# Kernel tuning notes

Hardware: AMD Instinct MI355X
Metric: run time of the kernel (lower is better)

Reference implementation:

```python
import jax, jax.numpy as jnp
import numpy as np

EPS = 1e-5
NUM_HEADS = 16

def rmsnorm(x, w=None, eps=EPS):
    y = x * jax.lax.rsqrt(jnp.mean(x * x, axis=-1, keepdims=True) + eps)
    return y if w is None else y * w

def act_quant(x):
    # per-token 8-bit absmax activation quantization (BitNet b1.58)
    scale = 127.0 / jnp.clip(jnp.max(jnp.abs(x), axis=-1, keepdims=True), 1e-5, None)
    return jnp.clip(jnp.round(x * scale), -128, 127) / scale

def weight_quant(w):
    # ternary (1.58-bit) absmean weight quantization
    scale = 1.0 / jnp.clip(jnp.mean(jnp.abs(w)), 1e-5, None)
    return jnp.clip(jnp.round(w * scale), -1, 1) / scale

def bit_linear(x, w):
    # BitLinear: RMSNorm -> STE-quantized activation @ STE-quantized ternary weight
    xn = rmsnorm(x)
    xq = xn + jax.lax.stop_gradient(act_quant(xn) - xn)
    wq = w + jax.lax.stop_gradient(weight_quant(w) - w)
    return xq @ wq.T

def hgrn_recurrence(i, logf):
    # elementwise gated linear recurrence: h_t = exp(logf_t) * h_{t-1} + i_t
    def step(h, xs):
        ii, ff = xs
        h = jnp.exp(ff) * h + ii
        return h, h
    B, T, D = i.shape
    _, o = jax.lax.scan(step, jnp.zeros((B, D), i.dtype),
                        (jnp.swapaxes(i, 0, 1), jnp.swapaxes(logf, 0, 1)))
    return jnp.swapaxes(o, 0, 1)  # [B, T, D]

def hgrn_bit_attention(x, w_i, w_f, w_g, w_o, g_norm_w):
    i = bit_linear(x, w_i)
    f = bit_linear(x, w_f)
    logf = jax.nn.log_sigmoid(f)
    i = jax.nn.silu(i) * (1.0 - jax.nn.sigmoid(f))  # swiglu(i, 1 - sigmoid(f))
    o = hgrn_recurrence(i, logf)
    g = bit_linear(x, w_g)
    B, T, D = o.shape
    oh = rmsnorm(o.reshape(B, T, NUM_HEADS, D // NUM_HEADS), g_norm_w)  # per-head RMSNorm
    o = oh.reshape(B, T, D) * g * jax.nn.sigmoid(g)  # swish gate (FusedRMSNormSwishGate)
    return bit_linear(o, w_o)

def setup_inputs() -> dict:
    key = jax.random.key(0)
    B, S_S, S_C, D = 4, 4096, 512, 2048
    ks = jax.random.split(key, 16)
    mk = lambda k: jax.random.normal(k, (D, D), jnp.float32) * 0.02
    return {
        "hidden_states": jax.random.normal(ks[0], (B, S_S, D), jnp.float32),
        "encoder_hidden_states": jax.random.normal(ks[1], (B, S_C, D), jnp.float32),
        "w_q": mk(ks[2]), "w_k": mk(ks[3]), "w_v": mk(ks[4]), "w_out": mk(ks[5]),
        "w_add_q": mk(ks[6]), "w_add_k": mk(ks[7]), "w_add_v": mk(ks[8]), "w_add_out": mk(ks[9]),
        "w_i": mk(ks[10]), "w_f": mk(ks[11]), "w_g": mk(ks[12]), "w_o": mk(ks[13]),
        "g_norm_w": jnp.ones((D // NUM_HEADS,), jnp.float32),
    }

def reference(hidden_states, encoder_hidden_states, w_q, w_k, w_v, w_out,
              w_add_q, w_add_k, w_add_v, w_add_out, w_i, w_f, w_g, w_o, g_norm_w):
    q_s = bit_linear(hidden_states, w_q)
    k_s = bit_linear(hidden_states, w_k)          # computed as in original; unused by attn
    v_s = bit_linear(hidden_states, w_v)          # computed as in original; unused by attn
    q_c = bit_linear(encoder_hidden_states, w_add_q)
    k_c = bit_linear(encoder_hidden_states, w_add_k)
    v_c = bit_linear(encoder_hidden_states, w_add_v)
    q_joint = jnp.concatenate([q_c, q_s], axis=1)  # context first, then stream
    attn_out = hgrn_bit_attention(q_joint, w_i, w_f, w_g, w_o, g_norm_w)
    len_c = encoder_hidden_states.shape[1]
    out_c, out_s = attn_out[:, :len_c, :], attn_out[:, len_c:, :]
    return (bit_linear(out_s, w_out), bit_linear(out_c, w_add_out))
```

## Files before the change

kernel.cpp:

```cpp
#include <hip/hip_runtime.h>
#include <math.h>
#include <stdint.h>

#define D2 2048

typedef int v4i __attribute__((ext_vector_type(4)));
typedef int v16i __attribute__((ext_vector_type(16)));

struct Ptrs8 { const float* p[8]; };
struct RowMap { int seg, jump, off; };

enum { QW_Q = 0, QW_OUT = 1, QW_ADDQ = 2, QW_ADDOUT = 3, QW_I = 4, QW_F = 5, QW_G = 6, QW_O = 7 };

__device__ __forceinline__ int rmap(RowMap m, int r) {
  return (r / m.seg) * m.jump + (r % m.seg) + m.off;
}

__device__ __forceinline__ void gload16(const void* g, void* l) {
  __builtin_amdgcn_global_load_lds((__attribute__((address_space(1))) void*)g,
                                   (__attribute__((address_space(3))) void*)l, 16, 0, 0);
}

__device__ __forceinline__ float fsig(float x) {
  return __builtin_amdgcn_rcpf(1.0f + __expf(-x));
}

__device__ __forceinline__ void gswz(int nM, int& mb, int& nb) {
  int bid = blockIdx.x;
  int wg = (bid & 7) * (nM << 1) + (bid >> 3);
  mb = wg >> 4;
  nb = wg & 15;
}

__global__ __launch_bounds__(256) void k_wabs(Ptrs8 wsrc, double* part) {
  int m = blockIdx.y;
  const float4* w4 = (const float4*)(wsrc.p[m] + (size_t)blockIdx.x * 4096 + threadIdx.x * 16);
  double s = 0.0;
#pragma unroll
  for (int j = 0; j < 4; ++j) {
    float4 v = w4[j];
    s += (double)fabsf(v.x) + (double)fabsf(v.y) + (double)fabsf(v.z) + (double)fabsf(v.w);
  }
#pragma unroll
  for (int o = 32; o; o >>= 1) s += __shfl_down(s, o);
  __shared__ double red[4];
  if ((threadIdx.x & 63) == 0) red[threadIdx.x >> 6] = s;
  __syncthreads();
  if (threadIdx.x == 0) part[(size_t)m * 1024 + blockIdx.x] = red[0] + red[1] + red[2] + red[3];
}

__global__ __launch_bounds__(256) void k_wmean(const double* part, double* wqs, float* wmul) {
  int m = blockIdx.x, t = threadIdx.x;
  const double* p = part + (size_t)m * 1024;
  double s = p[t] + p[t + 256] + p[t + 512] + p[t + 768];
#pragma unroll
  for (int o = 32; o; o >>= 1) s += __shfl_down(s, o);
  __shared__ double red[4];
  if ((t & 63) == 0) red[t >> 6] = s;
  __syncthreads();
  if (t == 0) {
    double mean = (red[0] + red[1] + red[2] + red[3]) * (1.0 / 4194304.0);
    double cl = mean > 1e-5 ? mean : 1e-5;
    wqs[m] = 1.0 / cl;
    wmul[m] = (float)cl;
  }
}

__global__ __launch_bounds__(256) void k_wquant(Ptrs8 wsrc, const double* wqs, int8_t* wq) {
  int m = blockIdx.y;
  double qs = wqs[m];
  size_t base = (size_t)blockIdx.x * 4096 + threadIdx.x * 16;
  const float4* w4 = (const float4*)(wsrc.p[m] + base);
  union { int8_t b[16]; int4 v; } u;
#pragma unroll
  for (int j = 0; j < 4; ++j) {
    float4 v = w4[j];
    float f[4] = {v.x, v.y, v.z, v.w};
#pragma unroll
    for (int c = 0; c < 4; ++c) {
      int q = (int)rint((double)f[c] * qs);
      q = q > 1 ? 1 : (q < -1 ? -1 : q);
      u.b[j * 4 + c] = (int8_t)q;
    }
  }
  *(int4*)(wq + (size_t)m * 4194304 + base) = u.v;
}

__global__ __launch_bounds__(256) void k_actq(const float* __restrict__ x, int8_t* __restrict__ q,
                                              float* __restrict__ inv) {
  int row = blockIdx.x, t = threadIdx.x;
  const float4* xr = (const float4*)(x + (size_t)row * D2);
  float4 a = xr[t * 2], b = xr[t * 2 + 1];
  float v[8] = {a.x, a.y, a.z, a.w, b.x, b.y, b.z, b.w};
  float ss = 0.f, ma = 0.f;
#pragma unroll
  for (int j = 0; j < 8; ++j) { ss += v[j] * v[j]; ma = fmaxf(ma, fabsf(v[j])); }
#pragma unroll
  for (int o = 32; o; o >>= 1) { ss += __shfl_down(ss, o); ma = fmaxf(ma, __shfl_down(ma, o)); }
  __shared__ float rs[4], rm[4], bc[2];
  if ((t & 63) == 0) { rs[t >> 6] = ss; rm[t >> 6] = ma; }
  __syncthreads();
  if (t == 0) {
    float S = rs[0] + rs[1] + rs[2] + rs[3];
    float M = fmaxf(fmaxf(rm[0], rm[1]), fmaxf(rm[2], rm[3]));
    float r = 1.0f / sqrtf(S * (1.0f / 2048.0f) + 1e-5f);
    float mx = fmaxf(M * r, 1e-5f);
    bc[0] = r;
    bc[1] = 127.0f / mx;
    inv[row] = mx * (1.0f / 127.0f);
  }
  __syncthreads();
  float r = bc[0], s = bc[1];
  union { int8_t b8[8]; int2 p2; } u;
#pragma unroll
  for (int j = 0; j < 8; ++j) {
    float xn = v[j] * r;
    int qq = (int)rintf(xn * s);
    qq = qq > 127 ? 127 : (qq < -128 ? -128 : qq);
    u.b8[j] = (int8_t)qq;
  }
  ((int2*)(q + (size_t)row * D2))[t] = u.p2;
}

#define SYNC_PIPE(N)                                          \
  do {                                                        \
    __builtin_amdgcn_sched_barrier(0);                        \
    asm volatile("s_waitcnt vmcnt(" #N ")" ::: "memory");     \
    __builtin_amdgcn_sched_barrier(0);                        \
    __builtin_amdgcn_s_barrier();                             \
    __builtin_amdgcn_sched_barrier(0);                        \
  } while (0)

__device__ __forceinline__ void gemm_mainloop(const int8_t* __restrict__ Aq,
                                              const int8_t* __restrict__ Wq, int ga0, int ga1,
                                              int n0, int t, int8_t* lds, v16i acc[2][2]) {
  const int wid = t >> 6, lane = t & 63;
  const int wr = wid >> 1, wc = wid & 1, am = lane & 31, g = lane >> 5;
  const int arow = t >> 2;
  const int achk = ((t & 3) ^ ((arow >> 1) & 3)) * 16;
  const int8_t* agp0 = Aq + (size_t)ga0 * 2048 + achk;
  const int8_t* agp1 = Aq + (size_t)ga1 * 2048 + achk;
  const int8_t* bgp0 = Wq + (size_t)(n0 + arow) * 2048 + achk;
  const int8_t* bgp1 = Wq + (size_t)(n0 + 64 + arow) * 2048 + achk;
  int8_t* A0 = lds;
  int8_t* B0 = lds + 8192;
  int8_t* A1 = lds + 16384;
  int8_t* B1 = lds + 24576;
  int8_t* A2 = lds + 32768;
  int8_t* B2 = lds + 40960;

#define STAGE(Ab, Bb)                                 \
  do {                                                \
    gload16(agp0, (Ab) + wid * 1024);                 \
    gload16(agp1, (Ab) + 4096 + wid * 1024);          \
    gload16(bgp0, (Bb) + wid * 1024);                 \
    gload16(bgp1, (Bb) + 4096 + wid * 1024);          \
    agp0 += 64; agp1 += 64; bgp0 += 64; bgp1 += 64;   \
  } while (0)

#define COMPUTE(Ab, Bb)                                                                     \
  do {                                                                                      \
    _Pragma("unroll") for (int kk = 0; kk < 2; ++kk) {                                      \
      v4i af[2], bf[2];                                                                     \
      _Pragma("unroll") for (int mi = 0; mi < 2; ++mi) {                                    \
        int r = wr * 64 + mi * 32 + am;                                                     \
        int slot = ((kk << 1) | g) ^ ((r >> 1) & 3);                                        \
        af[mi] = *(const v4i*)((Ab) + r * 64 + slot * 16);                                  \
        int rb = wc * 64 + mi * 32 + am;                                                    \
        int slotb = ((kk << 1) | g) ^ ((rb >> 1) & 3);                                      \
        bf[mi] = *(const v4i*)((Bb) + rb * 64 + slotb * 16);                                \
      }                                                                                     \
      _Pragma("unroll") for (int mi = 0; mi < 2; ++mi)                                      \
        _Pragma("unroll") for (int ni = 0; ni < 2; ++ni)                                    \
          acc[mi][ni] =                                                                     \
              __builtin_amdgcn_mfma_i32_32x32x32_i8(af[mi], bf[ni], acc[mi][ni], 0, 0, 0);  \
    }                                                                                       \
  } while (0)

  STAGE(A0, B0);
  STAGE(A1, B1);
  STAGE(A2, B2);
  SYNC_PIPE(8);
#pragma unroll 1
  for (int tt = 0; tt < 30; tt += 3) {
    COMPUTE(A0, B0);
    SYNC_PIPE(4);
    if (tt + 3 < 32) STAGE(A0, B0);
    COMPUTE(A1, B1);
    SYNC_PIPE(4);
    if (tt + 4 < 32) STAGE(A1, B1);
    COMPUTE(A2, B2);
    SYNC_PIPE(4);
    if (tt + 5 < 32) STAGE(A2, B2);
  }
  COMPUTE(A0, B0);
  SYNC_PIPE(0);
  COMPUTE(A1, B1);
#undef STAGE
#undef COMPUTE
}

__global__ __launch_bounds__(256) void k_gemm(const int8_t* __restrict__ Aq,
                                              const float* __restrict__ ainv,
                                              const int8_t* __restrict__ Wq,
                                              const float* __restrict__ wmul, int widx,
                                              float* __restrict__ C, RowMap inm, RowMap outm,
                                              int nM) {
  __shared__ __align__(16) int8_t lds[49152];
  int mb, nb;
  gswz(nM, mb, nb);
  int m0 = mb * 128, n0 = nb * 128;
  int t = threadIdx.x;
  int lane = t & 63, wid = t >> 6;
  int wr = wid >> 1, wc = wid & 1;
  int am = lane & 31, g = lane >> 5;
  int ga0 = rmap(inm, m0 + (t >> 2));
  int ga1 = rmap(inm, m0 + 64 + (t >> 2));

  v16i acc[2][2] = {};
  gemm_mainloop(Aq, Wq, ga0, ga1, n0, t, lds, acc);

  float wm = wmul[widx];
#pragma unroll
  for (int mi = 0; mi < 2; ++mi) {
#pragma unroll
    for (int q = 0; q < 16; ++q) {
      int rin = wr * 64 + mi * 32 + (q & 3) + ((q >> 2) * 8) + g * 4;
      int ra = rmap(inm, m0 + rin);
      int rc = rmap(outm, m0 + rin);
      float s = ainv[ra] * wm;
#pragma unroll
      for (int ni = 0; ni < 2; ++ni) {
        C[(size_t)rc * 2048 + n0 + wc * 64 + ni * 32 + am] = (float)acc[mi][ni][q] * s;
      }
    }
  }
}

__global__ __launch_bounds__(256) void k_gemm_f(const int8_t* __restrict__ Aq,
                                                const float* __restrict__ ainv,
                                                const int8_t* __restrict__ Wq,
                                                const float* __restrict__ wmul,
                                                float* __restrict__ IG, float* __restrict__ AD,
                                                int nM) {
  __shared__ __align__(16) int8_t lds[49152];
  int mb, nb;
  gswz(nM, mb, nb);
  int m0 = mb * 128, n0 = nb * 128;
  int t = threadIdx.x;
  int lane = t & 63, wid = t >> 6;
  int wr = wid >> 1, wc = wid & 1;
  int am = lane & 31, g = lane >> 5;
  int ga0 = m0 + (t >> 2);
  int ga1 = m0 + 64 + (t >> 2);

  v16i acc[2][2] = {};
  gemm_mainloop(Aq, Wq, ga0, ga1, n0, t, lds, acc);

  float wm = wmul[QW_F];
#pragma unroll
  for (int mi = 0; mi < 2; ++mi) {
#pragma unroll
    for (int q = 0; q < 16; ++q) {
      int rin = m0 + wr * 64 + mi * 32 + (q & 3) + ((q >> 2) * 8) + g * 4;
      float s = ainv[rin] * wm;
#pragma unroll
      for (int ni = 0; ni < 2; ++ni) {
        size_t idx = (size_t)rin * 2048 + n0 + wc * 64 + ni * 32 + am;
        float fval = (float)acc[mi][ni][q] * s;
        float iv = IG[idx];
        float a = fsig(fval);
        float si = iv * fsig(iv);
        IG[idx] = si * (1.0f - a);
        AD[idx] = a;
      }
    }
  }
}

__global__ __launch_bounds__(256) void k_rec1(const float* __restrict__ ig,
                                              const float* __restrict__ ad,
                                              float* __restrict__ chA, float* __restrict__ chH) {
  int tid = blockIdx.x * 256 + threadIdx.x;
  int chain = tid & 8191;
  int c = tid >> 13;
  int b = chain >> 11, d = chain & 2047;
  size_t base = ((size_t)b * 4608 + (size_t)c * 72) * 2048 + d;
  float h = 0.f, P = 1.f;
  for (int s = 0; s < 72; ++s) {
    float av = ad[base];
    float iv = ig[base];
    h = av * h + iv;
    P *= av;
    base += 2048;
  }
  chA[(size_t)c * 8192 + chain] = P;
  chH[(size_t)c * 8192 + chain] = h;
}

__global__ __launch_bounds__(256) void k_rec2(const float* __restrict__ chA,
                                              const float* __restrict__ chH,
                                              float* __restrict__ chC) {
  int chain = blockIdx.x * 256 + threadIdx.x;
  float carry = 0.f;
  for (int c = 0; c < 64; ++c) {
    chC[(size_t)c * 8192 + chain] = carry;
    carry = chA[(size_t)c * 8192 + chain] * carry + chH[(size_t)c * 8192 + chain];
  }
}

__global__ __launch_bounds__(256) void k_rec3(float* __restrict__ io, const float* __restrict__ ad,
                                              const float* __restrict__ chC) {
  int tid = blockIdx.x * 256 + threadIdx.x;
  int chain = tid & 8191;
  int c = tid >> 13;
  int b = chain >> 11, d = chain & 2047;
  size_t base = ((size_t)b * 4608 + (size_t)c * 72) * 2048 + d;
  float h = chC[(size_t)c * 8192 + chain];
  for (int s = 0; s < 72; ++s) {
    float av = ad[base];
    float iv = io[base];
    h = av * h + iv;
    io[base] = h;
    base += 2048;
  }
}

__global__ __launch_bounds__(256) void k_hnq(const float* __restrict__ o,
                                             const float* __restrict__ g,
                                             const float* __restrict__ gnw,
                                             int8_t* __restrict__ q, float* __restrict__ inv) {
  int row = blockIdx.x, t = threadIdx.x;
  size_t base = (size_t)row * D2 + (size_t)t * 8;
  float4 a = *(const float4*)(o + base);
  float4 b = *(const float4*)(o + base + 4);
  float v[8] = {a.x, a.y, a.z, a.w, b.x, b.y, b.z, b.w};
  float ss = 0.f;
#pragma unroll
  for (int j = 0; j < 8; ++j) ss += v[j] * v[j];
  ss += __shfl_xor(ss, 1);
  ss += __shfl_xor(ss, 2);
  ss += __shfl_xor(ss, 4);
  ss += __shfl_xor(ss, 8);
  float r = 1.0f / sqrtf(ss * (1.0f / 128.0f) + 1e-5f);
  float4 ga = *(const float4*)(g + base);
  float4 gb = *(const float4*)(g + base + 4);
  float gv[8] = {ga.x, ga.y, ga.z, ga.w, gb.x, gb.y, gb.z, gb.w};
  int j0 = (t & 15) * 8;
  float o2[8];
#pragma unroll
  for (int j = 0; j < 8; ++j) {
    float gg = gv[j];
    o2[j] = v[j] * r * gnw[j0 + j] * gg * fsig(gg);
  }
  float ss2 = 0.f, ma = 0.f;
#pragma unroll
  for (int j = 0; j < 8; ++j) { ss2 += o2[j] * o2[j]; ma = fmaxf(ma, fabsf(o2[j])); }
#pragma unroll
  for (int off = 32; off; off >>= 1) {
    ss2 += __shfl_down(ss2, off);
    ma = fmaxf(ma, __shfl_down(ma, off));
  }
  __shared__ float rs[4], rm[4], bc[2];
  if ((t & 63) == 0) { rs[t >> 6] = ss2; rm[t >> 6] = ma; }
  __syncthreads();
  if (t == 0) {
    float S = rs[0] + rs[1] + rs[2] + rs[3];
    float M = fmaxf(fmaxf(rm[0], rm[1]), fmaxf(rm[2], rm[3]));
    float rr = 1.0f / sqrtf(S * (1.0f / 2048.0f) + 1e-5f);
    float mx = fmaxf(M * rr, 1e-5f);
    bc[0] = rr;
    bc[1] = 127.0f / mx;
    inv[row] = mx * (1.0f / 127.0f);
  }
  __syncthreads();
  float rr = bc[0], s = bc[1];
  union { int8_t b8[8]; int2 p2; } u;
#pragma unroll
  for (int j = 0; j < 8; ++j) {
    float xn = o2[j] * rr;
    int qq = (int)rintf(xn * s);
    qq = qq > 127 ? 127 : (qq < -128 ? -128 : qq);
    u.b8[j] = (int8_t)qq;
  }
  ((int2*)(q + (size_t)row * D2))[t] = u.p2;
}

extern "C" void kernel_launch(void* const* d_in, const int* in_sizes, int n_in,
                              void* d_out, int out_size, void* d_ws, size_t ws_size,
                              hipStream_t stream) {
  const float* hid = (const float*)d_in[0];
  const float* enc = (const float*)d_in[1];
  const float* gnw = (const float*)d_in[14];
  Ptrs8 wp;
  wp.p[QW_Q] = (const float*)d_in[2];
  wp.p[QW_OUT] = (const float*)d_in[5];
  wp.p[QW_ADDQ] = (const float*)d_in[6];
  wp.p[QW_ADDOUT] = (const float*)d_in[9];
  wp.p[QW_I] = (const float*)d_in[10];
  wp.p[QW_F] = (const float*)d_in[11];
  wp.p[QW_G] = (const float*)d_in[12];
  wp.p[QW_O] = (const float*)d_in[13];
  float* out = (float*)d_out;

  char* ws = (char*)d_ws;
  float* bufA = (float*)ws;
  float* bufB = bufA + 37748736;
  int8_t* actq = (int8_t*)(bufB + 37748736);
  int8_t* wq = actq + 37748736;
  float* ainv = (float*)(wq + 33554432);
  double* wpart = (double*)(ainv + 18432);
  double* wqs = wpart + 8192;
  float* wmul = (float*)(wqs + 8);
  float* chA = wmul + 8;
  float* chH = chA + 524288;
  float* chC = chH + 524288;
  if (ws_size < 379723872ULL) return;

  RowMap idm{0x40000000, 0, 0};
  RowMap seqm{4096, 4608, 512};
  RowMap encm{512, 4608, 0};

  k_wabs<<<dim3(1024, 8), 256, 0, stream>>>(wp, wpart);
  k_wmean<<<8, 256, 0, stream>>>(wpart, wqs, wmul);
  k_wquant<<<dim3(1024, 8), 256, 0, stream>>>(wp, wqs, wq);
  k_actq<<<16384, 256, 0, stream>>>(hid, actq, ainv);
  k_actq<<<2048, 256, 0, stream>>>(enc, actq + (size_t)16384 * 2048, ainv + 16384);
  k_gemm<<<128 * 16, 256, 0, stream>>>(actq, ainv, wq + (size_t)QW_Q * 4194304, wmul, QW_Q,
                                       bufA, idm, seqm, 128);
  k_gemm<<<16 * 16, 256, 0, stream>>>(actq + (size_t)16384 * 2048, ainv + 16384,
                                      wq + (size_t)QW_ADDQ * 4194304, wmul, QW_ADDQ, bufA,
                                      idm, encm, 16);
  k_actq<<<18432, 256, 0, stream>>>(bufA, actq, ainv);
  k_gemm<<<144 * 16, 256, 0, stream>>>(actq, ainv, wq + (size_t)QW_I * 4194304, wmul, QW_I,
                                       bufA, idm, idm, 144);
  k_gemm<<<144 * 16, 256, 0, stream>>>(actq, ainv, wq + (size_t)QW_G * 4194304, wmul, QW_G,
                                       out, idm, idm, 144);
  k_gemm_f<<<144 * 16, 256, 0, stream>>>(actq, ainv, wq + (size_t)QW_F * 4194304, wmul,
                                         bufA, bufB, 144);
  k_rec1<<<2048, 256, 0, stream>>>(bufA, bufB, chA, chH);
  k_rec2<<<32, 256, 0, stream>>>(chA, chH, chC);
  k_rec3<<<2048, 256, 0, stream>>>(bufA, bufB, chC);
  k_hnq<<<18432, 256, 0, stream>>>(bufA, out, gnw, actq, ainv);
  k_gemm<<<144 * 16, 256, 0, stream>>>(actq, ainv, wq + (size_t)QW_O * 4194304, wmul, QW_O,
                                       bufB, idm, idm, 144);
  k_actq<<<18432, 256, 0, stream>>>(bufB, actq, ainv);
  k_gemm<<<128 * 16, 256, 0, stream>>>(actq, ainv, wq + (size_t)QW_OUT * 4194304, wmul,
                                       QW_OUT, out, seqm, idm, 128);
  k_gemm<<<16 * 16, 256, 0, stream>>>(actq, ainv, wq + (size_t)QW_ADDOUT * 4194304, wmul,
                                      QW_ADDOUT, out + (size_t)33554432, encm, idm, 16);
}
```

Baseline: 1.117 ms.

## Use 256x256 int8 MFMA GEMM tiles with 512-thread blocks for large projections

Adds a 256x256-tile int8 GEMM with 8 waves per block, a double-buffered 64-deep K pipeline split into half-stage loads, an XOR-swizzled fragment layout, and s_setprio around the MFMA phases. The large projections (Q, I, G, F, O, OUT) move to it, while the small encoder GEMMs keep the 128x128 kernel. The larger tile raises arithmetic intensity and cuts global and LDS traffic per MFMA. In exchange it uses 64KB LDS and more accumulator registers per block, which lowers occupancy, and the grid shrinks to 512-576 blocks, which can hurt wave balance across CUs.

```diff
diff --git a/kernel.cpp b/kernel.cpp
--- a/kernel.cpp
+++ b/kernel.cpp
@@ -25,11 +25,107 @@
   return __builtin_amdgcn_rcpf(1.0f + __expf(-x));
 }
 
-__device__ __forceinline__ void gswz(int nM, int& mb, int& nb) {
+
+__device__ __forceinline__ int frag_off(int r) {
+  int rp = r >> 1, p = r & 1;
+  return rp * 128 + ((p ^ ((rp >> 2) & 1)) << 6) + ((rp & 3) << 4);
+}
+
+__device__ __forceinline__ void gswz256(int nMt, int& mb, int& nb) {
   int bid = blockIdx.x;
-  int wg = (bid & 7) * (nM << 1) + (bid >> 3);
-  mb = wg >> 4;
-  nb = wg & 15;
+  int wg = (bid & 7) * nMt + (bid >> 3);
+  mb = wg >> 3;
+  nb = wg & 7;
+}
+
+#define BAR()                              \
+  __builtin_amdgcn_sched_barrier(0);       \
+  __builtin_amdgcn_s_barrier();            \
+  __builtin_amdgcn_sched_barrier(0)
+
+#define VMC(N)                                                        \
+  __builtin_amdgcn_sched_barrier(0);                                  \
+  asm volatile("s_waitcnt vmcnt(%0)" ::"i"(N) : "memory");            \
+  __builtin_amdgcn_sched_barrier(0)
+
+#define PH_MFMA(kk)                                                                         \
+  __builtin_amdgcn_s_setprio(1);                                                            \
+  _Pragma("unroll") for (int mi = 0; mi < 4; ++mi)                                          \
+    _Pragma("unroll") for (int ni = 0; ni < 2; ++ni)                                        \
+        acc[mi][ni] =                                                                       \
+            __builtin_amdgcn_mfma_i32_32x32x32_i8(fa[mi][kk], fb[ni][kk], acc[mi][ni], 0, 0, 0); \
+  __builtin_amdgcn_s_setprio(0)
+
+#define GROUP(BOFF, DOSTAGE, VMN)                                                           \
+  do {                                                                                      \
+    const int8_t* ABp = lds + (BOFF);                                                       \
+    const int8_t* BBp = lds + 32768 + (BOFF);                                               \
+    v4i fa[4][2], fb[2][2];                                                                 \
+    _Pragma("unroll") for (int mi = 0; mi < 4; ++mi)                                        \
+      _Pragma("unroll") for (int kk = 0; kk < 2; ++kk)                                      \
+          fa[mi][kk] = *(const v4i*)(ABp + (aoff[mi] ^ ((((kk) << 1) | hi) << 4)));         \
+    _Pragma("unroll") for (int ni = 0; ni < 2; ++ni)                                        \
+      _Pragma("unroll") for (int kk = 0; kk < 2; ++kk)                                      \
+          fb[ni][kk] = *(const v4i*)(BBp + (boff[ni] ^ ((((kk) << 1) | hi) << 4)));         \
+    BAR();                                                                                  \
+    if (DOSTAGE) {                                                                          \
+      gload16(sa0 + kS, lds + (BOFF) + wid * 1024);                                         \
+      gload16(sb0 + kS, lds + 32768 + (BOFF) + wid * 1024);                                 \
+    }                                                                                       \
+    PH_MFMA(0);                                                                             \
+    BAR();                                                                                  \
+    if (DOSTAGE) {                                                                          \
+      gload16(sa1 + kS, lds + (BOFF) + 8192 + wid * 1024);                                  \
+      gload16(sb1 + kS, lds + 32768 + (BOFF) + 8192 + wid * 1024);                          \
+      kS += 64;                                                                             \
+    }                                                                                       \
+    PH_MFMA(1);                                                                             \
+    VMC(VMN);                                                                               \
+    BAR();                                                                                  \
+  } while (0)
+
+__device__ __forceinline__ void mainloop256(const int8_t* __restrict__ Aq,
+                                            const int8_t* __restrict__ Wq, RowMap inm, int m0,
+                                            int n0, int t, int8_t* lds, v16i acc[4][2]) {
+  const int wid = t >> 6, lane = t & 63, am = lane & 31, hi = lane >> 5;
+  const int wr = wid >> 2, wc = wid & 3;
+  const int rp_l = t >> 3, sl = t & 7;
+  const int8_t *sa0, *sa1, *sb0, *sb1;
+  {
+    int rp = rp_l, s0 = sl ^ (rp & 7), p = s0 >> 2, c = s0 & 3;
+    sa0 = Aq + (size_t)rmap(inm, m0 + 2 * rp + p) * 2048 + c * 16;
+    sb0 = Wq + (size_t)(n0 + 2 * rp + p) * 2048 + c * 16;
+  }
+  {
+    int rp = 64 + rp_l, s0 = sl ^ (rp & 7), p = s0 >> 2, c = s0 & 3;
+    sa1 = Aq + (size_t)rmap(inm, m0 + 2 * rp + p) * 2048 + c * 16;
+    sb1 = Wq + (size_t)(n0 + 2 * rp + p) * 2048 + c * 16;
+  }
+  int aoff[4], boff[2];
+#pragma unroll
+  for (int mi = 0; mi < 4; ++mi) aoff[mi] = frag_off(wr * 128 + mi * 32 + am);
+#pragma unroll
+  for (int ni = 0; ni < 2; ++ni) boff[ni] = frag_off(wc * 64 + ni * 32 + am);
+
+  int kS = 0;
+  gload16(sa0 + 0, lds + wid * 1024);
+  gload16(sb0 + 0, lds + 32768 + wid * 1024);
+  gload16(sa1 + 0, lds + 8192 + wid * 1024);
+  gload16(sb1 + 0, lds + 32768 + 8192 + wid * 1024);
+  gload16(sa0 + 64, lds + 16384 + wid * 1024);
+  gload16(sb0 + 64, lds + 49152 + wid * 1024);
+  gload16(sa1 + 64, lds + 16384 + 8192 + wid * 1024);
+  gload16(sb1 + 64, lds + 49152 + 8192 + wid * 1024);
+  kS = 128;
+  VMC(4);
+  BAR();
+#pragma unroll 1
+  for (int it = 0; it < 15; ++it) {
+    GROUP(0, 1, 4);
+    GROUP(16384, 1, 4);
+  }
+  GROUP(0, 0, 0);
+  GROUP(16384, 0, 0);
 }
 
 __global__ __launch_bounds__(256) void k_wabs(Ptrs8 wsrc, double* part) {
@@ -122,6 +218,82 @@
   ((int2*)(q + (size_t)row * D2))[t] = u.p2;
 }
 
+__global__ __launch_bounds__(512, 2) void k_gemm256(const int8_t* __restrict__ Aq,
+                                                    const float* __restrict__ ainv,
+                                                    const int8_t* __restrict__ Wq,
+                                                    const float* __restrict__ wmul, int widx,
+                                                    float* __restrict__ C, RowMap inm,
+                                                    RowMap outm, int nMt) {
+  __shared__ __align__(16) int8_t lds[65536];
+  int mb, nb;
+  gswz256(nMt, mb, nb);
+  int m0 = mb * 256, n0 = nb * 256;
+  int t = threadIdx.x;
+  v16i acc[4][2] = {};
+  mainloop256(Aq, Wq, inm, m0, n0, t, lds, acc);
+  int wid = t >> 6, lane = t & 63, am = lane & 31, hi = lane >> 5;
+  int wr = wid >> 2, wc = wid & 3;
+  float wm = wmul[widx];
+#pragma unroll
+  for (int mi = 0; mi < 4; ++mi) {
+#pragma unroll
+    for (int q = 0; q < 16; ++q) {
+      int rin = wr * 128 + mi * 32 + (q & 3) + ((q >> 2) * 8) + hi * 4;
+      int ra = rmap(inm, m0 + rin);
+      int rc = rmap(outm, m0 + rin);
+      float s = ainv[ra] * wm;
+#pragma unroll
+      for (int ni = 0; ni < 2; ++ni) {
+        C[(size_t)rc * 2048 + n0 + wc * 64 + ni * 32 + am] = (float)acc[mi][ni][q] * s;
+      }
+    }
+  }
+}
+
+__global__ __launch_bounds__(512, 2) void k_gemm256_f(const int8_t* __restrict__ Aq,
+                                                      const float* __restrict__ ainv,
+                                                      const int8_t* __restrict__ Wq,
+                                                      const float* __restrict__ wmul,
+                                                      float* __restrict__ IG,
+                                                      float* __restrict__ AD, int nMt) {
+  __shared__ __align__(16) int8_t lds[65536];
+  int mb, nb;
+  gswz256(nMt, mb, nb);
+  int m0 = mb * 256, n0 = nb * 256;
+  int t = threadIdx.x;
+  v16i acc[4][2] = {};
+  RowMap idm{0x40000000, 0, 0};
+  mainloop256(Aq, Wq, idm, m0, n0, t, lds, acc);
+  int wid = t >> 6, lane = t & 63, am = lane & 31, hi = lane >> 5;
+  int wr = wid >> 2, wc = wid & 3;
+  float wm = wmul[QW_F];
+#pragma unroll
+  for (int mi = 0; mi < 4; ++mi) {
+#pragma unroll
+    for (int q = 0; q < 16; ++q) {
+      int rin = m0 + wr * 128 + mi * 32 + (q & 3) + ((q >> 2) * 8) + hi * 4;
+      float s = ainv[rin] * wm;
+#pragma unroll
+      for (int ni = 0; ni < 2; ++ni) {
+        size_t idx = (size_t)rin * 2048 + n0 + wc * 64 + ni * 32 + am;
+        float fval = (float)acc[mi][ni][q] * s;
+        float iv = IG[idx];
+        float a = fsig(fval);
+        float si = iv * fsig(iv);
+        IG[idx] = si * (1.0f - a);
+        AD[idx] = a;
+      }
+    }
+  }
+}
+
+__device__ __forceinline__ void gswz128(int nM, int& mb, int& nb) {
+  int bid = blockIdx.x;
+  int wg = (bid & 7) * (nM << 1) + (bid >> 3);
+  mb = wg >> 4;
+  nb = wg & 15;
+}
+
 #define SYNC_PIPE(N)                                          \
   do {                                                        \
     __builtin_amdgcn_sched_barrier(0);                        \
@@ -131,9 +303,9 @@
     __builtin_amdgcn_sched_barrier(0);                        \
   } while (0)
 
-__device__ __forceinline__ void gemm_mainloop(const int8_t* __restrict__ Aq,
-                                              const int8_t* __restrict__ Wq, int ga0, int ga1,
-                                              int n0, int t, int8_t* lds, v16i acc[2][2]) {
+__device__ __forceinline__ void gemm_mainloop128(const int8_t* __restrict__ Aq,
+                                                 const int8_t* __restrict__ Wq, int ga0, int ga1,
+                                                 int n0, int t, int8_t* lds, v16i acc[2][2]) {
   const int wid = t >> 6, lane = t & 63;
   const int wr = wid >> 1, wc = wid & 1, am = lane & 31, g = lane >> 5;
   const int arow = t >> 2;
@@ -149,7 +321,7 @@
   int8_t* A2 = lds + 32768;
   int8_t* B2 = lds + 40960;
 
-#define STAGE(Ab, Bb)                                 \
+#define STAGE128(Ab, Bb)                              \
   do {                                                \
     gload16(agp0, (Ab) + wid * 1024);                 \
     gload16(agp1, (Ab) + 4096 + wid * 1024);          \
@@ -158,7 +330,7 @@
     agp0 += 64; agp1 += 64; bgp0 += 64; bgp1 += 64;   \
   } while (0)
 
-#define COMPUTE(Ab, Bb)                                                                     \
+#define COMPUTE128(Ab, Bb)                                                                  \
   do {                                                                                      \
     _Pragma("unroll") for (int kk = 0; kk < 2; ++kk) {                                      \
       v4i af[2], bf[2];                                                                     \
@@ -177,27 +349,27 @@
     }                                                                                       \
   } while (0)
 
-  STAGE(A0, B0);
-  STAGE(A1, B1);
-  STAGE(A2, B2);
+  STAGE128(A0, B0);
+  STAGE128(A1, B1);
+  STAGE128(A2, B2);
   SYNC_PIPE(8);
 #pragma unroll 1
   for (int tt = 0; tt < 30; tt += 3) {
-    COMPUTE(A0, B0);
+    COMPUTE128(A0, B0);
     SYNC_PIPE(4);
-    if (tt + 3 < 32) STAGE(A0, B0);
-    COMPUTE(A1, B1);
+    if (tt + 3 < 32) STAGE128(A0, B0);
+    COMPUTE128(A1, B1);
     SYNC_PIPE(4);
-    if (tt + 4 < 32) STAGE(A1, B1);
-    COMPUTE(A2, B2);
+    if (tt + 4 < 32) STAGE128(A1, B1);
+    COMPUTE128(A2, B2);
     SYNC_PIPE(4);
-    if (tt + 5 < 32) STAGE(A2, B2);
-  }
-  COMPUTE(A0, B0);
+    if (tt + 5 < 32) STAGE128(A2, B2);
+  }
+  COMPUTE128(A0, B0);
   SYNC_PIPE(0);
-  COMPUTE(A1, B1);
-#undef STAGE
-#undef COMPUTE
+  COMPUTE128(A1, B1);
+#undef STAGE128
+#undef COMPUTE128
 }
 
 __global__ __launch_bounds__(256) void k_gemm(const int8_t* __restrict__ Aq,
@@ -208,7 +380,7 @@
                                               int nM) {
   __shared__ __align__(16) int8_t lds[49152];
   int mb, nb;
-  gswz(nM, mb, nb);
+  gswz128(nM, mb, nb);
   int m0 = mb * 128, n0 = nb * 128;
   int t = threadIdx.x;
   int lane = t & 63, wid = t >> 6;
@@ -218,7 +390,7 @@
   int ga1 = rmap(inm, m0 + 64 + (t >> 2));
 
   v16i acc[2][2] = {};
-  gemm_mainloop(Aq, Wq, ga0, ga1, n0, t, lds, acc);
+  gemm_mainloop128(Aq, Wq, ga0, ga1, n0, t, lds, acc);
 
   float wm = wmul[widx];
 #pragma unroll
@@ -232,47 +404,6 @@
 #pragma unroll
       for (int ni = 0; ni < 2; ++ni) {
         C[(size_t)rc * 2048 + n0 + wc * 64 + ni * 32 + am] = (float)acc[mi][ni][q] * s;
-      }
-    }
-  }
-}
-
-__global__ __launch_bounds__(256) void k_gemm_f(const int8_t* __restrict__ Aq,
-                                                const float* __restrict__ ainv,
-                                                const int8_t* __restrict__ Wq,
-                                                const float* __restrict__ wmul,
-                                                float* __restrict__ IG, float* __restrict__ AD,
-                                                int nM) {
-  __shared__ __align__(16) int8_t lds[49152];
-  int mb, nb;
-  gswz(nM, mb, nb);
-  int m0 = mb * 128, n0 = nb * 128;
-  int t = threadIdx.x;
-  int lane = t & 63, wid = t >> 6;
-  int wr = wid >> 1, wc = wid & 1;
-  int am = lane & 31, g = lane >> 5;
-  int ga0 = m0 + (t >> 2);
-  int ga1 = m0 + 64 + (t >> 2);
-
-  v16i acc[2][2] = {};
-  gemm_mainloop(Aq, Wq, ga0, ga1, n0, t, lds, acc);
-
-  float wm = wmul[QW_F];
-#pragma unroll
-  for (int mi = 0; mi < 2; ++mi) {
-#pragma unroll
-    for (int q = 0; q < 16; ++q) {
-      int rin = m0 + wr * 64 + mi * 32 + (q & 3) + ((q >> 2) * 8) + g * 4;
-      float s = ainv[rin] * wm;
-#pragma unroll
-      for (int ni = 0; ni < 2; ++ni) {
-        size_t idx = (size_t)rin * 2048 + n0 + wc * 64 + ni * 32 + am;
-        float fval = (float)acc[mi][ni][q] * s;
-        float iv = IG[idx];
-        float a = fsig(fval);
-        float si = iv * fsig(iv);
-        IG[idx] = si * (1.0f - a);
-        AD[idx] = a;
       }
     }
   }
@@ -426,27 +557,27 @@
   k_wquant<<<dim3(1024, 8), 256, 0, stream>>>(wp, wqs, wq);
   k_actq<<<16384, 256, 0, stream>>>(hid, actq, ainv);
   k_actq<<<2048, 256, 0, stream>>>(enc, actq + (size_t)16384 * 2048, ainv + 16384);
-  k_gemm<<<128 * 16, 256, 0, stream>>>(actq, ainv, wq + (size_t)QW_Q * 4194304, wmul, QW_Q,
-                                       bufA, idm, seqm, 128);
+  k_gemm256<<<64 * 8, 512, 0, stream>>>(actq, ainv, wq + (size_t)QW_Q * 4194304, wmul, QW_Q,
+                                        bufA, idm, seqm, 64);
   k_gemm<<<16 * 16, 256, 0, stream>>>(actq + (size_t)16384 * 2048, ainv + 16384,
                                       wq + (size_t)QW_ADDQ * 4194304, wmul, QW_ADDQ, bufA,
                                       idm, encm, 16);
   k_actq<<<18432, 256, 0, stream>>>(bufA, actq, ainv);
-  k_gemm<<<144 * 16, 256, 0, stream>>>(actq, ainv, wq + (size_t)QW_I * 4194304, wmul, QW_I,
-                                       bufA, idm, idm, 144);
-  k_gemm<<<144 * 16, 256, 0, stream>>>(actq, ainv, wq + (size_t)QW_G * 4194304, wmul, QW_G,
-                                       out, idm, idm, 144);
-  k_gemm_f<<<144 * 16, 256, 0, stream>>>(actq, ainv, wq + (size_t)QW_F * 4194304, wmul,
-                                         bufA, bufB, 144);
+  k_gemm256<<<72 * 8, 512, 0, stream>>>(actq, ainv, wq + (size_t)QW_I * 4194304, wmul, QW_I,
+                                        bufA, idm, idm, 72);
+  k_gemm256<<<72 * 8, 512, 0, stream>>>(actq, ainv, wq + (size_t)QW_G * 4194304, wmul, QW_G,
+                                        out, idm, idm, 72);
+  k_gemm256_f<<<72 * 8, 512, 0, stream>>>(actq, ainv, wq + (size_t)QW_F * 4194304, wmul,
+                                          bufA, bufB, 72);
   k_rec1<<<2048, 256, 0, stream>>>(bufA, bufB, chA, chH);
   k_rec2<<<32, 256, 0, stream>>>(chA, chH, chC);
   k_rec3<<<2048, 256, 0, stream>>>(bufA, bufB, chC);
   k_hnq<<<18432, 256, 0, stream>>>(bufA, out, gnw, actq, ainv);
-  k_gemm<<<144 * 16, 256, 0, stream>>>(actq, ainv, wq + (size_t)QW_O * 4194304, wmul, QW_O,
-                                       bufB, idm, idm, 144);
+  k_gemm256<<<72 * 8, 512, 0, stream>>>(actq, ainv, wq + (size_t)QW_O * 4194304, wmul, QW_O,
+                                        bufB, idm, idm, 72);
   k_actq<<<18432, 256, 0, stream>>>(bufB, actq, ainv);
-  k_gemm<<<128 * 16, 256, 0, stream>>>(actq, ainv, wq + (size_t)QW_OUT * 4194304, wmul,
-                                       QW_OUT, out, seqm, idm, 128);
+  k_gemm256<<<64 * 8, 512, 0, stream>>>(actq, ainv, wq + (size_t)QW_OUT * 4194304, wmul,
+                                        QW_OUT, out, seqm, idm, 64);
   k_gemm<<<16 * 16, 256, 0, stream>>>(actq, ainv, wq + (size_t)QW_ADDOUT * 4194304, wmul,
                                       QW_ADDOUT, out + (size_t)33554432, encm, idm, 16);
 }
```

Result: slower. 1.206 ms (+7.9%).

## Fuse the i and f gate GEMMs into one kernel sharing A tiles

Applied to the files above, without the earlier changes.

Combines the W_i and W_f projections into a single GEMM kernel that loads each activation tile once and runs two sets of MFMA accumulators against both weight tiles. The i-gate output no longer goes through memory in fp32 to be re-read by the f-gate epilogue, and one kernel launch and one activation pass are removed. In exchange the kernel uses 72KB of LDS and twice the accumulator registers per block, which lowers occupancy.

```diff
diff --git a/kernel.cpp b/kernel.cpp
--- a/kernel.cpp
+++ b/kernel.cpp
@@ -131,9 +131,9 @@
     __builtin_amdgcn_sched_barrier(0);                        \
   } while (0)
 
-__device__ __forceinline__ void gemm_mainloop(const int8_t* __restrict__ Aq,
-                                              const int8_t* __restrict__ Wq, int ga0, int ga1,
-                                              int n0, int t, int8_t* lds, v16i acc[2][2]) {
+__device__ __forceinline__ void gemm_mainloop128(const int8_t* __restrict__ Aq,
+                                                 const int8_t* __restrict__ Wq, int ga0, int ga1,
+                                                 int n0, int t, int8_t* lds, v16i acc[2][2]) {
   const int wid = t >> 6, lane = t & 63;
   const int wr = wid >> 1, wc = wid & 1, am = lane & 31, g = lane >> 5;
   const int arow = t >> 2;
@@ -149,7 +149,7 @@
   int8_t* A2 = lds + 32768;
   int8_t* B2 = lds + 40960;
 
-#define STAGE(Ab, Bb)                                 \
+#define STAGE128(Ab, Bb)                              \
   do {                                                \
     gload16(agp0, (Ab) + wid * 1024);                 \
     gload16(agp1, (Ab) + 4096 + wid * 1024);          \
@@ -158,7 +158,7 @@
     agp0 += 64; agp1 += 64; bgp0 += 64; bgp1 += 64;   \
   } while (0)
 
-#define COMPUTE(Ab, Bb)                                                                     \
+#define COMPUTE128(Ab, Bb)                                                                  \
   do {                                                                                      \
     _Pragma("unroll") for (int kk = 0; kk < 2; ++kk) {                                      \
       v4i af[2], bf[2];                                                                     \
@@ -177,27 +177,27 @@
     }                                                                                       \
   } while (0)
 
-  STAGE(A0, B0);
-  STAGE(A1, B1);
-  STAGE(A2, B2);
+  STAGE128(A0, B0);
+  STAGE128(A1, B1);
+  STAGE128(A2, B2);
   SYNC_PIPE(8);
 #pragma unroll 1
   for (int tt = 0; tt < 30; tt += 3) {
-    COMPUTE(A0, B0);
+    COMPUTE128(A0, B0);
     SYNC_PIPE(4);
-    if (tt + 3 < 32) STAGE(A0, B0);
-    COMPUTE(A1, B1);
+    if (tt + 3 < 32) STAGE128(A0, B0);
+    COMPUTE128(A1, B1);
     SYNC_PIPE(4);
-    if (tt + 4 < 32) STAGE(A1, B1);
-    COMPUTE(A2, B2);
+    if (tt + 4 < 32) STAGE128(A1, B1);
+    COMPUTE128(A2, B2);
     SYNC_PIPE(4);
-    if (tt + 5 < 32) STAGE(A2, B2);
-  }
-  COMPUTE(A0, B0);
+    if (tt + 5 < 32) STAGE128(A2, B2);
+  }
+  COMPUTE128(A0, B0);
   SYNC_PIPE(0);
-  COMPUTE(A1, B1);
-#undef STAGE
-#undef COMPUTE
+  COMPUTE128(A1, B1);
+#undef STAGE128
+#undef COMPUTE128
 }
 
 __global__ __launch_bounds__(256) void k_gemm(const int8_t* __restrict__ Aq,
@@ -218,7 +218,7 @@
   int ga1 = rmap(inm, m0 + 64 + (t >> 2));
 
   v16i acc[2][2] = {};
-  gemm_mainloop(Aq, Wq, ga0, ga1, n0, t, lds, acc);
+  gemm_mainloop128(Aq, Wq, ga0, ga1, n0, t, lds, acc);
 
   float wm = wmul[widx];
 #pragma unroll
@@ -237,41 +237,106 @@
   }
 }
 
-__global__ __launch_bounds__(256) void k_gemm_f(const int8_t* __restrict__ Aq,
-                                                const float* __restrict__ ainv,
-                                                const int8_t* __restrict__ Wq,
-                                                const float* __restrict__ wmul,
-                                                float* __restrict__ IG, float* __restrict__ AD,
-                                                int nM) {
-  __shared__ __align__(16) int8_t lds[49152];
+__global__ __launch_bounds__(256) void k_gemm_if(const int8_t* __restrict__ Aq,
+                                                 const float* __restrict__ ainv,
+                                                 const int8_t* __restrict__ Wi,
+                                                 const int8_t* __restrict__ Wf,
+                                                 const float* __restrict__ wmul,
+                                                 float* __restrict__ IG, float* __restrict__ AD,
+                                                 int nM) {
+  __shared__ __align__(16) int8_t lds[73728];
   int mb, nb;
   gswz(nM, mb, nb);
   int m0 = mb * 128, n0 = nb * 128;
   int t = threadIdx.x;
-  int lane = t & 63, wid = t >> 6;
-  int wr = wid >> 1, wc = wid & 1;
-  int am = lane & 31, g = lane >> 5;
-  int ga0 = m0 + (t >> 2);
-  int ga1 = m0 + 64 + (t >> 2);
-
-  v16i acc[2][2] = {};
-  gemm_mainloop(Aq, Wq, ga0, ga1, n0, t, lds, acc);
-
-  float wm = wmul[QW_F];
+  const int wid = t >> 6, lane = t & 63;
+  const int wr = wid >> 1, wc = wid & 1, am = lane & 31, g = lane >> 5;
+  const int arow = t >> 2;
+  const int achk = ((t & 3) ^ ((arow >> 1) & 3)) * 16;
+  const int8_t* agp0 = Aq + (size_t)(m0 + arow) * 2048 + achk;
+  const int8_t* agp1 = Aq + (size_t)(m0 + 64 + arow) * 2048 + achk;
+  const int8_t* bip0 = Wi + (size_t)(n0 + arow) * 2048 + achk;
+  const int8_t* bip1 = Wi + (size_t)(n0 + 64 + arow) * 2048 + achk;
+  const int8_t* bfp0 = Wf + (size_t)(n0 + arow) * 2048 + achk;
+  const int8_t* bfp1 = Wf + (size_t)(n0 + 64 + arow) * 2048 + achk;
+
+  v16i acci[2][2] = {};
+  v16i accf[2][2] = {};
+
+#define STAGE_IF(B)                                                                   \
+  do {                                                                                \
+    gload16(agp0, lds + (B) + wid * 1024);                                            \
+    gload16(agp1, lds + (B) + 4096 + wid * 1024);                                     \
+    gload16(bip0, lds + (B) + 8192 + wid * 1024);                                     \
+    gload16(bip1, lds + (B) + 12288 + wid * 1024);                                    \
+    gload16(bfp0, lds + (B) + 16384 + wid * 1024);                                    \
+    gload16(bfp1, lds + (B) + 20480 + wid * 1024);                                    \
+    agp0 += 64; agp1 += 64; bip0 += 64; bip1 += 64; bfp0 += 64; bfp1 += 64;           \
+  } while (0)
+
+#define COMPUTE_IF(B)                                                                       \
+  do {                                                                                      \
+    _Pragma("unroll") for (int kk = 0; kk < 2; ++kk) {                                      \
+      v4i af[2], bfi[2], bff[2];                                                            \
+      _Pragma("unroll") for (int mi = 0; mi < 2; ++mi) {                                    \
+        int r = wr * 64 + mi * 32 + am;                                                     \
+        int slot = ((kk << 1) | g) ^ ((r >> 1) & 3);                                        \
+        af[mi] = *(const v4i*)(lds + (B) + r * 64 + slot * 16);                             \
+      }                                                                                     \
+      _Pragma("unroll") for (int ni = 0; ni < 2; ++ni) {                                    \
+        int rb = wc * 64 + ni * 32 + am;                                                    \
+        int slotb = ((kk << 1) | g) ^ ((rb >> 1) & 3);                                      \
+        bfi[ni] = *(const v4i*)(lds + (B) + 8192 + rb * 64 + slotb * 16);                   \
+        bff[ni] = *(const v4i*)(lds + (B) + 16384 + rb * 64 + slotb * 16);                  \
+      }                                                                                     \
+      _Pragma("unroll") for (int mi = 0; mi < 2; ++mi)                                      \
+        _Pragma("unroll") for (int ni = 0; ni < 2; ++ni) {                                  \
+          acci[mi][ni] =                                                                    \
+              __builtin_amdgcn_mfma_i32_32x32x32_i8(af[mi], bfi[ni], acci[mi][ni], 0, 0, 0);\
+          accf[mi][ni] =                                                                    \
+              __builtin_amdgcn_mfma_i32_32x32x32_i8(af[mi], bff[ni], accf[mi][ni], 0, 0, 0);\
+        }                                                                                   \
+    }                                                                                       \
+  } while (0)
+
+  STAGE_IF(0);
+  STAGE_IF(24576);
+  STAGE_IF(49152);
+  SYNC_PIPE(12);
+#pragma unroll 1
+  for (int tt = 0; tt < 30; tt += 3) {
+    COMPUTE_IF(0);
+    SYNC_PIPE(6);
+    if (tt + 3 < 32) STAGE_IF(0);
+    COMPUTE_IF(24576);
+    SYNC_PIPE(6);
+    if (tt + 4 < 32) STAGE_IF(24576);
+    COMPUTE_IF(49152);
+    SYNC_PIPE(6);
+    if (tt + 5 < 32) STAGE_IF(49152);
+  }
+  COMPUTE_IF(0);
+  SYNC_PIPE(0);
+  COMPUTE_IF(24576);
+#undef STAGE_IF
+#undef COMPUTE_IF
+
+  float wmi = wmul[QW_I], wmf = wmul[QW_F];
 #pragma unroll
   for (int mi = 0; mi < 2; ++mi) {
 #pragma unroll
     for (int q = 0; q < 16; ++q) {
       int rin = m0 + wr * 64 + mi * 32 + (q & 3) + ((q >> 2) * 8) + g * 4;
-      float s = ainv[rin] * wm;
+      float si = ainv[rin] * wmi;
+      float sf = ainv[rin] * wmf;
 #pragma unroll
       for (int ni = 0; ni < 2; ++ni) {
         size_t idx = (size_t)rin * 2048 + n0 + wc * 64 + ni * 32 + am;
-        float fval = (float)acc[mi][ni][q] * s;
-        float iv = IG[idx];
-        float a = fsig(fval);
-        float si = iv * fsig(iv);
-        IG[idx] = si * (1.0f - a);
+        float iv = (float)acci[mi][ni][q] * si;
+        float fv = (float)accf[mi][ni][q] * sf;
+        float a = fsig(fv);
+        float s2 = iv * fsig(iv);
+        IG[idx] = s2 * (1.0f - a);
         AD[idx] = a;
       }
     }
@@ -432,12 +497,10 @@
                                       wq + (size_t)QW_ADDQ * 4194304, wmul, QW_ADDQ, bufA,
                                       idm, encm, 16);
   k_actq<<<18432, 256, 0, stream>>>(bufA, actq, ainv);
-  k_gemm<<<144 * 16, 256, 0, stream>>>(actq, ainv, wq + (size_t)QW_I * 4194304, wmul, QW_I,
-                                       bufA, idm, idm, 144);
+  k_gemm_if<<<144 * 16, 256, 0, stream>>>(actq, ainv, wq + (size_t)QW_I * 4194304,
+                                          wq + (size_t)QW_F * 4194304, wmul, bufA, bufB, 144);
   k_gemm<<<144 * 16, 256, 0, stream>>>(actq, ainv, wq + (size_t)QW_G * 4194304, wmul, QW_G,
                                        out, idm, idm, 144);
-  k_gemm_f<<<144 * 16, 256, 0, stream>>>(actq, ainv, wq + (size_t)QW_F * 4194304, wmul,
-                                         bufA, bufB, 144);
   k_rec1<<<2048, 256, 0, stream>>>(bufA, bufB, chA, chH);
   k_rec2<<<32, 256, 0, stream>>>(chA, chH, chC);
   k_rec3<<<2048, 256, 0, stream>>>(bufA, bufB, chC);
```

Result: faster. 1.025 ms (-8.2%).
